# Kernel tuning notes

Measured on AMD Instinct MI355X. Metric: run time of the kernel, lower is better.

## Reference

```python
import jax, jax.numpy as jnp
import numpy as np

N, C, S = 2, 512, 256
SCALE = 2.0

def setup_inputs() -> dict:
    key = jax.random.key(0)
    kq, kk, kv = jax.random.split(key, 3)
    q = jax.random.normal(kq, (N, C, S), dtype=jnp.float32)
    k = jax.random.normal(kk, (N, C, S), dtype=jnp.float32)
    v = jax.random.normal(kv, (N, C, S), dtype=jnp.float32)
    return {"q": q, "k": k, "v": v}

def reference(q, k, v):
    # q: (N,C,S) -> (N,C,1,S); k: (N,C,S) -> (N,1,C,S)
    # weights[n,c,d] = -sum_s |k[n,d,s] - q[n,c,s]| / scale
    diff = jnp.abs(k[:, None, :, :] - q[:, :, None, :])  # (N,C,C,S)
    weights = -(diff / SCALE).sum(axis=-1)               # (N,C,C)
    weights = jax.nn.softmax(weights, axis=-1)
    rep = jnp.einsum('ncd,nds->ncs', weights, v)         # (N,C,S)
    return rep
```

## Files before the change

kernel.cpp:

```cpp
#include <hip/hip_runtime.h>
#include <hip/hip_bf16.h>


constexpr int N_ = 2;
constexpr int C_ = 512;
constexpr int S_ = 256;
constexpr int TC = 8;
constexpr int NW = 4;
constexpr int DSPLIT = 8;
constexpr int DH  = C_ / DSPLIT;
constexpr int DPW = DH / NW;

constexpr size_t PO_SZ = (size_t)N_ * C_ * DSPLIT * S_;
constexpr size_t ST_SZ = (size_t)N_ * C_ * DSPLIT;

template <int CTRL, int ROW_MASK>
__device__ __forceinline__ float dpp_add(float x) {
    int yi = __builtin_amdgcn_update_dpp(0, __float_as_int(x), CTRL, ROW_MASK, 0xf, true);
    return x + __int_as_float(yi);
}
template <int CTRL, int ROW_MASK>
__device__ __forceinline__ float dpp_max(float x) {
    int yi = __builtin_amdgcn_update_dpp(__float_as_int(x), __float_as_int(x), CTRL, ROW_MASK, 0xf, false);
    return fmaxf(x, __int_as_float(yi));
}
__device__ __forceinline__ float dpp_reduce_halves(float x) {
    x = dpp_add<0x111, 0xf>(x);
    x = dpp_add<0x112, 0xf>(x);
    x = dpp_add<0x114, 0xf>(x);
    x = dpp_add<0x118, 0xf>(x);
    x = dpp_add<0x142, 0xa>(x);
    return x;
}
__device__ __forceinline__ float wave_sum_bcast(float x) {
    x = dpp_reduce_halves(x);
    x = dpp_add<0x143, 0xc>(x);
    return __int_as_float(__builtin_amdgcn_readlane(__float_as_int(x), 63));
}
__device__ __forceinline__ float wave_max_bcast(float x) {
    x = dpp_max<0x111, 0xf>(x);
    x = dpp_max<0x112, 0xf>(x);
    x = dpp_max<0x114, 0xf>(x);
    x = dpp_max<0x118, 0xf>(x);
    x = dpp_max<0x142, 0xa>(x);
    x = dpp_max<0x143, 0xc>(x);
    return __int_as_float(__builtin_amdgcn_readlane(__float_as_int(x), 63));
}

__global__ __launch_bounds__(256, 4)
void laplace_attn_main(const float* __restrict__ q,
                       const float* __restrict__ k,
                       const float* __restrict__ v,
                       float* __restrict__ ws) {
    constexpr int per_n = (C_ / TC) * DSPLIT;
    const int b    = blockIdx.x;
    const int n    = b / per_n;
    const int r    = b - n * per_n;
    const int half = r % DSPLIT;
    const int c0   = (r / DSPLIT) * TC;
    const int tid  = threadIdx.x;
    const int w    = tid >> 6;
    const int lane = tid & 63;

    const float* kbase = k + (size_t)n * C_ * S_;
    const float* vbase = v + (size_t)n * C_ * S_;

    float* po = ws;
    float* pm = ws + PO_SZ;
    float* pl = pm + ST_SZ;

    __shared__ float4 wt[DH][2];
    __shared__ float4 accs[NW][TC][64];

    const int h = lane >> 5;
    const int j = lane & 31;
    float4 qa[TC], qb[TC];
    #pragma unroll
    for (int c = 0; c < TC; ++c) {
        const float4* qr = (const float4*)(q + ((size_t)n * C_ + c0 + c) * S_);
        qa[c] = qr[2 * j];
        qb[c] = qr[2 * j + 1];
    }

    const int dw0 = half * DH + w * DPW;
    const float* kw = kbase + (size_t)dw0 * S_;

    #pragma unroll 2
    for (int g2 = 0; g2 < DPW; g2 += 2) {
        const float4* rp = (const float4*)(kw + (size_t)(g2 + h) * S_ + j * 8);
        const float4 ka = rp[0];
        const float4 kb = rp[1];
        float vals[TC];
        #pragma unroll
        for (int c = 0; c < TC; ++c) {
            float p = fabsf(ka.x - qa[c].x) + fabsf(ka.y - qa[c].y)
                    + fabsf(ka.z - qa[c].z) + fabsf(ka.w - qa[c].w)
                    + fabsf(kb.x - qb[c].x) + fabsf(kb.y - qb[c].y)
                    + fabsf(kb.z - qb[c].z) + fabsf(kb.w - qb[c].w);
            vals[c] = dpp_reduce_halves(p);
        }
        if ((lane & 31) == 31) {
            const int row = w * DPW + g2 + h;
            wt[row][0] = make_float4(-0.5f * vals[0], -0.5f * vals[1],
                                     -0.5f * vals[2], -0.5f * vals[3]);
            wt[row][1] = make_float4(-0.5f * vals[4], -0.5f * vals[5],
                                     -0.5f * vals[6], -0.5f * vals[7]);
        }
    }
    __syncthreads();

    {
        float* wtf = (float*)wt;
        #pragma unroll
        for (int cc = 0; cc < 2; ++cc) {
            const int c = 2 * w + cc;
            const float x = wtf[lane * 8 + c];
            const float m = wave_max_bcast(x);
            const float e = __expf(x - m);
            const float l = wave_sum_bcast(e);
            wtf[lane * 8 + c] = e;
            if (lane == 0) {
                const size_t sidx = ((size_t)n * C_ + c0 + c) * DSPLIT + half;
                pm[sidx] = m;
                pl[sidx] = l;
            }
        }
    }
    __syncthreads();

    float4 acc[TC];
    #pragma unroll
    for (int c = 0; c < TC; ++c) acc[c] = make_float4(0.f, 0.f, 0.f, 0.f);

    const float4* v4 = (const float4*)(vbase + (size_t)dw0 * S_);
    #pragma unroll 4
    for (int dd = 0; dd < DPW; ++dd) {
        const float4 vv = v4[dd * 64 + lane];
        const float4 w0 = wt[w * DPW + dd][0];
        const float4 w1 = wt[w * DPW + dd][1];
        acc[0].x += w0.x * vv.x; acc[0].y += w0.x * vv.y;
        acc[0].z += w0.x * vv.z; acc[0].w += w0.x * vv.w;
        acc[1].x += w0.y * vv.x; acc[1].y += w0.y * vv.y;
        acc[1].z += w0.y * vv.z; acc[1].w += w0.y * vv.w;
        acc[2].x += w0.z * vv.x; acc[2].y += w0.z * vv.y;
        acc[2].z += w0.z * vv.z; acc[2].w += w0.z * vv.w;
        acc[3].x += w0.w * vv.x; acc[3].y += w0.w * vv.y;
        acc[3].z += w0.w * vv.z; acc[3].w += w0.w * vv.w;
        acc[4].x += w1.x * vv.x; acc[4].y += w1.x * vv.y;
        acc[4].z += w1.x * vv.z; acc[4].w += w1.x * vv.w;
        acc[5].x += w1.y * vv.x; acc[5].y += w1.y * vv.y;
        acc[5].z += w1.y * vv.z; acc[5].w += w1.y * vv.w;
        acc[6].x += w1.z * vv.x; acc[6].y += w1.z * vv.y;
        acc[6].z += w1.z * vv.z; acc[6].w += w1.z * vv.w;
        acc[7].x += w1.w * vv.x; acc[7].y += w1.w * vv.y;
        acc[7].z += w1.w * vv.z; acc[7].w += w1.w * vv.w;
    }
    #pragma unroll
    for (int c = 0; c < TC; ++c) accs[w][c][lane] = acc[c];
    __syncthreads();

    #pragma unroll
    for (int cc = 0; cc < 2; ++cc) {
        const int c = w + NW * cc;
        const float4 a0 = accs[0][c][lane];
        const float4 a1 = accs[1][c][lane];
        const float4 a2 = accs[2][c][lane];
        const float4 a3 = accs[3][c][lane];
        float4 o;
        o.x = (a0.x + a1.x) + (a2.x + a3.x);
        o.y = (a0.y + a1.y) + (a2.y + a3.y);
        o.z = (a0.z + a1.z) + (a2.z + a3.z);
        o.w = (a0.w + a1.w) + (a2.w + a3.w);
        const size_t oidx = (((size_t)n * C_ + c0 + c) * DSPLIT + half) * S_;
        ((float4*)(po + oidx))[lane] = o;
    }
}

__global__ __launch_bounds__(64)
void laplace_attn_combine(const float* __restrict__ ws,
                          float* __restrict__ out) {
    const int b    = blockIdx.x;
    const int lane = threadIdx.x;

    const float* po = ws;
    const float* pm = ws + PO_SZ;
    const float* pl = pm + ST_SZ;

    float m[DSPLIT], l[DSPLIT];
    #pragma unroll
    for (int hh = 0; hh < DSPLIT; ++hh) {
        m[hh] = pm[(size_t)b * DSPLIT + hh];
        l[hh] = pl[(size_t)b * DSPLIT + hh];
    }
    float M = m[0];
    #pragma unroll
    for (int hh = 1; hh < DSPLIT; ++hh) M = fmaxf(M, m[hh]);
    float den = 0.f, a[DSPLIT];
    #pragma unroll
    for (int hh = 0; hh < DSPLIT; ++hh) { a[hh] = __expf(m[hh] - M); den += a[hh] * l[hh]; }
    const float inv = 1.f / den;

    float4 rsum = make_float4(0.f, 0.f, 0.f, 0.f);
    #pragma unroll
    for (int hh = 0; hh < DSPLIT; ++hh) {
        const float4 o = ((const float4*)(po + ((size_t)b * DSPLIT + hh) * S_))[lane];
        rsum.x += a[hh] * o.x;
        rsum.y += a[hh] * o.y;
        rsum.z += a[hh] * o.z;
        rsum.w += a[hh] * o.w;
    }
    float4 rr;
    rr.x = rsum.x * inv; rr.y = rsum.y * inv;
    rr.z = rsum.z * inv; rr.w = rsum.w * inv;
    ((float4*)(out + (size_t)b * S_))[lane] = rr;
}

extern "C" void kernel_launch(void* const* d_in, const int* in_sizes, int n_in,
                              void* d_out, int out_size, void* d_ws, size_t ws_size,
                              hipStream_t stream) {
    const float* q = (const float*)d_in[0];
    const float* k = (const float*)d_in[1];
    const float* v = (const float*)d_in[2];
    float* out = (float*)d_out;
    float* ws  = (float*)d_ws;

    laplace_attn_main<<<dim3(N_ * (C_ / TC) * DSPLIT), dim3(256), 0, stream>>>(q, k, v, ws);
    laplace_attn_combine<<<dim3(N_ * C_), dim3(64), 0, stream>>>(ws, out);
}
```

Measured before the change: 81.13 us.

## Halve query tile, drop LDS partial reduction, prefetch K/V rows

Halves the query rows per block from 8 to 4, which doubles the grid and raises the occupancy hint in the launch bounds. Each wave now writes its own partial output to global memory instead of reducing the four waves' partials through shared memory. The combine kernel then sums 32 partials per row instead of 8. The K and V loops also load the next row into registers before computing on the current one. The aim is more parallelism and less LDS traffic and synchronisation, at the cost of four times more workspace traffic, re-reading K and V for twice as many blocks, and a larger workspace requirement.

```diff
diff --git a/kernel.cpp b/kernel.cpp
--- a/kernel.cpp
+++ b/kernel.cpp
@@ -5,13 +5,14 @@
 constexpr int N_ = 2;
 constexpr int C_ = 512;
 constexpr int S_ = 256;
-constexpr int TC = 8;
+constexpr int TC = 4;
 constexpr int NW = 4;
 constexpr int DSPLIT = 8;
 constexpr int DH  = C_ / DSPLIT;
 constexpr int DPW = DH / NW;
-
-constexpr size_t PO_SZ = (size_t)N_ * C_ * DSPLIT * S_;
+constexpr int NPART = DSPLIT * NW;
+
+constexpr size_t PO_SZ = (size_t)N_ * C_ * NPART * S_;
 constexpr size_t ST_SZ = (size_t)N_ * C_ * DSPLIT;
 
 template <int CTRL, int ROW_MASK>
@@ -47,7 +48,7 @@
     return __int_as_float(__builtin_amdgcn_readlane(__float_as_int(x), 63));
 }
 
-__global__ __launch_bounds__(256, 4)
+__global__ __launch_bounds__(256, 6)
 void laplace_attn_main(const float* __restrict__ q,
                        const float* __restrict__ k,
                        const float* __restrict__ v,
@@ -69,8 +70,7 @@
     float* pm = ws + PO_SZ;
     float* pl = pm + ST_SZ;
 
-    __shared__ float4 wt[DH][2];
-    __shared__ float4 accs[NW][TC][64];
+    __shared__ float4 wt[DH];
 
     const int h = lane >> 5;
     const int j = lane & 31;
@@ -83,96 +83,79 @@
     }
 
     const int dw0 = half * DH + w * DPW;
-    const float* kw = kbase + (size_t)dw0 * S_;
-
-    #pragma unroll 2
-    for (int g2 = 0; g2 < DPW; g2 += 2) {
-        const float4* rp = (const float4*)(kw + (size_t)(g2 + h) * S_ + j * 8);
-        const float4 ka = rp[0];
-        const float4 kb = rp[1];
-        float vals[TC];
+
+    {
+        const float4* rp = (const float4*)(kbase + (size_t)(dw0 + h) * S_) + 2 * j;
+        float4 ka = rp[0];
+        float4 kb = rp[1];
         #pragma unroll
-        for (int c = 0; c < TC; ++c) {
-            float p = fabsf(ka.x - qa[c].x) + fabsf(ka.y - qa[c].y)
-                    + fabsf(ka.z - qa[c].z) + fabsf(ka.w - qa[c].w)
-                    + fabsf(kb.x - qb[c].x) + fabsf(kb.y - qb[c].y)
-                    + fabsf(kb.z - qb[c].z) + fabsf(kb.w - qb[c].w);
-            vals[c] = dpp_reduce_halves(p);
-        }
-        if ((lane & 31) == 31) {
-            const int row = w * DPW + g2 + h;
-            wt[row][0] = make_float4(-0.5f * vals[0], -0.5f * vals[1],
-                                     -0.5f * vals[2], -0.5f * vals[3]);
-            wt[row][1] = make_float4(-0.5f * vals[4], -0.5f * vals[5],
-                                     -0.5f * vals[6], -0.5f * vals[7]);
+        for (int g2 = 0; g2 < DPW; g2 += 2) {
+            const float4* rpn = (g2 + 2 < DPW) ? rp + 2 * (S_ / 4) : rp;
+            float4 kan = rpn[0];
+            float4 kbn = rpn[1];
+
+            float vals[TC];
+            #pragma unroll
+            for (int c = 0; c < TC; ++c) {
+                float p = fabsf(ka.x - qa[c].x) + fabsf(ka.y - qa[c].y)
+                        + fabsf(ka.z - qa[c].z) + fabsf(ka.w - qa[c].w)
+                        + fabsf(kb.x - qb[c].x) + fabsf(kb.y - qb[c].y)
+                        + fabsf(kb.z - qb[c].z) + fabsf(kb.w - qb[c].w);
+                vals[c] = dpp_reduce_halves(p);
+            }
+            if ((lane & 31) == 31) {
+                wt[w * DPW + g2 + h] = make_float4(-0.5f * vals[0], -0.5f * vals[1],
+                                                   -0.5f * vals[2], -0.5f * vals[3]);
+            }
+            ka = kan; kb = kbn; rp = rpn;
         }
     }
     __syncthreads();
 
     {
         float* wtf = (float*)wt;
+        const float x = wtf[lane * TC + w];
+        const float m = wave_max_bcast(x);
+        const float e = __expf(x - m);
+        const float l = wave_sum_bcast(e);
+        wtf[lane * TC + w] = e;
+        if (lane == 0) {
+            const size_t sidx = ((size_t)n * C_ + c0 + w) * DSPLIT + half;
+            pm[sidx] = m;
+            pl[sidx] = l;
+        }
+    }
+    __syncthreads();
+
+    float4 acc[TC];
+    #pragma unroll
+    for (int c = 0; c < TC; ++c) acc[c] = make_float4(0.f, 0.f, 0.f, 0.f);
+
+    {
+        const float4* vp = (const float4*)(vbase + (size_t)dw0 * S_) + lane;
+        float4 vv = vp[0];
         #pragma unroll
-        for (int cc = 0; cc < 2; ++cc) {
-            const int c = 2 * w + cc;
-            const float x = wtf[lane * 8 + c];
-            const float m = wave_max_bcast(x);
-            const float e = __expf(x - m);
-            const float l = wave_sum_bcast(e);
-            wtf[lane * 8 + c] = e;
-            if (lane == 0) {
-                const size_t sidx = ((size_t)n * C_ + c0 + c) * DSPLIT + half;
-                pm[sidx] = m;
-                pl[sidx] = l;
-            }
+        for (int dd = 0; dd < DPW; ++dd) {
+            const float4* vpn = (dd + 1 < DPW) ? vp + (S_ / 4) : vp;
+            float4 vvn = vpn[0];
+            const float4 ww = wt[w * DPW + dd];
+            acc[0].x += ww.x * vv.x; acc[0].y += ww.x * vv.y;
+            acc[0].z += ww.x * vv.z; acc[0].w += ww.x * vv.w;
+            acc[1].x += ww.y * vv.x; acc[1].y += ww.y * vv.y;
+            acc[1].z += ww.y * vv.z; acc[1].w += ww.y * vv.w;
+            acc[2].x += ww.z * vv.x; acc[2].y += ww.z * vv.y;
+            acc[2].z += ww.z * vv.z; acc[2].w += ww.z * vv.w;
+            acc[3].x += ww.w * vv.x; acc[3].y += ww.w * vv.y;
+            acc[3].z += ww.w * vv.z; acc[3].w += ww.w * vv.w;
+            vv = vvn; vp = vpn;
         }
     }
-    __syncthreads();
-
-    float4 acc[TC];
-    #pragma unroll
-    for (int c = 0; c < TC; ++c) acc[c] = make_float4(0.f, 0.f, 0.f, 0.f);
-
-    const float4* v4 = (const float4*)(vbase + (size_t)dw0 * S_);
-    #pragma unroll 4
-    for (int dd = 0; dd < DPW; ++dd) {
-        const float4 vv = v4[dd * 64 + lane];
-        const float4 w0 = wt[w * DPW + dd][0];
-        const float4 w1 = wt[w * DPW + dd][1];
-        acc[0].x += w0.x * vv.x; acc[0].y += w0.x * vv.y;
-        acc[0].z += w0.x * vv.z; acc[0].w += w0.x * vv.w;
-        acc[1].x += w0.y * vv.x; acc[1].y += w0.y * vv.y;
-        acc[1].z += w0.y * vv.z; acc[1].w += w0.y * vv.w;
-        acc[2].x += w0.z * vv.x; acc[2].y += w0.z * vv.y;
-        acc[2].z += w0.z * vv.z; acc[2].w += w0.z * vv.w;
-        acc[3].x += w0.w * vv.x; acc[3].y += w0.w * vv.y;
-        acc[3].z += w0.w * vv.z; acc[3].w += w0.w * vv.w;
-        acc[4].x += w1.x * vv.x; acc[4].y += w1.x * vv.y;
-        acc[4].z += w1.x * vv.z; acc[4].w += w1.x * vv.w;
-        acc[5].x += w1.y * vv.x; acc[5].y += w1.y * vv.y;
-        acc[5].z += w1.y * vv.z; acc[5].w += w1.y * vv.w;
-        acc[6].x += w1.z * vv.x; acc[6].y += w1.z * vv.y;
-        acc[6].z += w1.z * vv.z; acc[6].w += w1.z * vv.w;
-        acc[7].x += w1.w * vv.x; acc[7].y += w1.w * vv.y;
-        acc[7].z += w1.w * vv.z; acc[7].w += w1.w * vv.w;
-    }
-    #pragma unroll
-    for (int c = 0; c < TC; ++c) accs[w][c][lane] = acc[c];
-    __syncthreads();
-
-    #pragma unroll
-    for (int cc = 0; cc < 2; ++cc) {
-        const int c = w + NW * cc;
-        const float4 a0 = accs[0][c][lane];
-        const float4 a1 = accs[1][c][lane];
-        const float4 a2 = accs[2][c][lane];
-        const float4 a3 = accs[3][c][lane];
-        float4 o;
-        o.x = (a0.x + a1.x) + (a2.x + a3.x);
-        o.y = (a0.y + a1.y) + (a2.y + a3.y);
-        o.z = (a0.z + a1.z) + (a2.z + a3.z);
-        o.w = (a0.w + a1.w) + (a2.w + a3.w);
-        const size_t oidx = (((size_t)n * C_ + c0 + c) * DSPLIT + half) * S_;
-        ((float4*)(po + oidx))[lane] = o;
+
+    #pragma unroll
+    for (int c = 0; c < TC; ++c) {
+        const size_t row  = (size_t)n * C_ + c0 + c;
+        const size_t oidx = ((row * DSPLIT + half) * NW + w) * S_;
+        ((float4*)(po + oidx))[lane] = acc[c];
     }
 }
 
@@ -202,12 +185,13 @@
 
     float4 rsum = make_float4(0.f, 0.f, 0.f, 0.f);
     #pragma unroll
-    for (int hh = 0; hh < DSPLIT; ++hh) {
-        const float4 o = ((const float4*)(po + ((size_t)b * DSPLIT + hh) * S_))[lane];
-        rsum.x += a[hh] * o.x;
-        rsum.y += a[hh] * o.y;
-        rsum.z += a[hh] * o.z;
-        rsum.w += a[hh] * o.w;
+    for (int p2 = 0; p2 < NPART; ++p2) {
+        const float wgt = a[p2 / NW];
+        const float4 o = ((const float4*)(po + ((size_t)b * NPART + p2) * S_))[lane];
+        rsum.x += wgt * o.x;
+        rsum.y += wgt * o.y;
+        rsum.z += wgt * o.z;
+        rsum.w += wgt * o.w;
     }
     float4 rr;
     rr.x = rsum.x * inv; rr.y = rsum.y * inv;
```

New measurement: 169.2 us. 2.09x slower.
